# Optimization experiments

Hardware: AMD Instinct MI355X
Metric: run time of the kernel (lower is better)

The kernel has to match this reference:

```python
import jax, jax.numpy as jnp
import numpy as np
import math

HIDDEN = 256

def setup_inputs() -> dict:
    key = jax.random.key(0)
    ks = jax.random.split(key, 4)
    x = jax.random.normal(ks[0], (64, 1024, 32), dtype=jnp.float32)
    Wq = jax.random.normal(ks[1], (32, HIDDEN), dtype=jnp.float32) * (1.0 / math.sqrt(32))
    Wk = jax.random.normal(ks[2], (32, HIDDEN), dtype=jnp.float32) * (1.0 / math.sqrt(32))
    Wv = jax.random.normal(ks[3], (32, HIDDEN), dtype=jnp.float32) * (1.0 / math.sqrt(32))
    bq = jnp.zeros((HIDDEN,), jnp.float32)
    bk = jnp.zeros((HIDDEN,), jnp.float32)
    bv = jnp.zeros((HIDDEN,), jnp.float32)
    return {"x": x, "Wq": Wq, "bq": bq, "Wk": Wk, "bk": bk, "Wv": Wv, "bv": bv}

def reference(x, Wq, bq, Wk, bk, Wv, bv):
    # per-sample single-head attention; softmax FIRST, then divide by sqrt(hidden)
    Q = jnp.einsum('bsi,ih->bsh', x, Wq) + bq  # [B,S,H]
    K = jnp.einsum('bsi,ih->bsh', x, Wk) + bk
    V = jnp.einsum('bsi,ih->bsh', x, Wv) + bv
    scores = jnp.einsum('bqh,bkh->bqk', Q, K)  # [B,S,S]
    attn = jax.nn.softmax(scores, axis=-1) / jnp.sqrt(jnp.float32(Q.shape[-1]))
    Z = jnp.einsum('bqk,bkh->bqh', attn, V)
    return Z
```

## Files before the change

kernel.cpp:

```cpp
#include <hip/hip_runtime.h>
#include <math.h>

#define NB   64
#define SEQ  1024
#define DIN  32
#define HID  256
#define QT   128
#define KT   64
#define NKT  (SEQ/KT)
#define LOG2E 1.4426950408889634f

typedef float        f32x16 __attribute__((ext_vector_type(16)));
typedef short        s16x8  __attribute__((ext_vector_type(8)));
typedef _Float16     f16x8  __attribute__((ext_vector_type(8)));
typedef unsigned int u32x4v __attribute__((ext_vector_type(4)));
typedef unsigned int u32x2v __attribute__((ext_vector_type(2)));

#define MFMA32(A,B,C)  __builtin_amdgcn_mfma_f32_32x32x16_bf16(A,B,C,0,0,0)
#define MFMA32H(A,B,C) __builtin_amdgcn_mfma_f32_32x32x16_f16(A,B,C,0,0,0)

#define OFF_WVT  4224
#define OFF_A    24576
#define OFF_T    (OFF_A + 64*16*8192)
#define WS_NEED  ((size_t)OFF_T + 64*16*4096)

#define SETB(g,p) (((g)*2+(p))*12288)
#define ATS_OFF   49152
#define SMEM_SZ   (ATS_OFF + 4224)

__device__ __forceinline__ float ex2(float v) {
  return __builtin_amdgcn_exp2f(v);
}
__device__ __forceinline__ unsigned pk_bf16(float lo, float hi) {
  unsigned r;
  asm("v_cvt_pk_bf16_f32 %0, %1, %2" : "=v"(r) : "v"(lo), "v"(hi));
  return r;
}
__device__ __forceinline__ unsigned pkh(float a, float b) {
  return __builtin_bit_cast(unsigned, __builtin_amdgcn_cvt_pkrtz(a, b));
}
__device__ __forceinline__ void plswap(unsigned &vdst, unsigned &vsrc) {
  u32x2v r = __builtin_amdgcn_permlane32_swap(vdst, vsrc, false, false);
  vdst = r[0]; vsrc = r[1];
}
__device__ __forceinline__ float cross_max(float v) {
  u32x2v r = __builtin_amdgcn_permlane32_swap(__float_as_uint(v), __float_as_uint(v), false, false);
  return fmaxf(__uint_as_float(r[0]), __uint_as_float(r[1]));
}
__device__ __forceinline__ float cross_add(float v) {
  u32x2v r = __builtin_amdgcn_permlane32_swap(__float_as_uint(v), __float_as_uint(v), false, false);
  return __uint_as_float(r[0]) + __uint_as_float(r[1]);
}
__device__ __forceinline__ s16x8 frag4(unsigned a, unsigned b, unsigned c, unsigned d) {
  u32x4v t; t[0]=a; t[1]=b; t[2]=c; t[3]=d;
  return __builtin_bit_cast(s16x8, t);
}
__device__ __forceinline__ f16x8 frag4h(unsigned a, unsigned b, unsigned c, unsigned d) {
  u32x4v t; t[0]=a; t[1]=b; t[2]=c; t[3]=d;
  return __builtin_bit_cast(f16x8, t);
}
__device__ __forceinline__ f16x8 ldh(const void* p) {
  return __builtin_bit_cast(f16x8, *(const u32x4v*)p);
}
__device__ __forceinline__ unsigned bf16_hi_bits(float f) {
  unsigned ux = __float_as_uint(f);
  return (ux + 0x7fffu + ((ux >> 16) & 1u)) >> 16;
}
__device__ __forceinline__ unsigned pack_h2(float a, float b) {
  _Float16 ha = (_Float16)a, hb = (_Float16)b;
  return (unsigned)__builtin_bit_cast(unsigned short, ha) |
         ((unsigned)__builtin_bit_cast(unsigned short, hb) << 16);
}


__global__ __launch_bounds__(256) void pack2_kernel(
    const float* __restrict__ x,
    const float* __restrict__ Wq, const float* __restrict__ Wk,
    const float* __restrict__ bq, const float* __restrict__ Wv,
    char* __restrict__ ws) {
  __shared__ float xs[64 * 33];
  const int bid = blockIdx.x;
  const int t   = threadIdx.x;
  if (bid < 1024) {
    const int b = bid >> 4, kt = bid & 15;
    {
      const int r = t >> 2, c = (t & 3) * 8;
      const float* src = x + ((size_t)(b*SEQ + kt*KT + r))*DIN + c;
      float4 v0 = *(const float4*)src, v1 = *(const float4*)(src + 4);
      float* d = xs + r*33 + c;
      d[0]=v0.x; d[1]=v0.y; d[2]=v0.z; d[3]=v0.w;
      d[4]=v1.x; d[5]=v1.y; d[6]=v1.z; d[7]=v1.w;
    }
    __syncthreads();
    const int l = t & 63, f = t >> 6;
    const int w = l >> 5, lq = l & 31;
    {
      const int row = ((f&2)?32:0) + lq;
      const int d0  = ((f&1)?16:0) + 8*w;
      const float* vsrc = xs + row*33 + d0;
      unsigned hi[4], lo[4];
      #pragma unroll
      for (int j = 0; j < 4; ++j) {
        float a = vsrc[2*j], c2 = vsrc[2*j+1];
        _Float16 ha = (_Float16)a, hb = (_Float16)c2;
        hi[j] = (unsigned)__builtin_bit_cast(unsigned short, ha) |
                ((unsigned)__builtin_bit_cast(unsigned short, hb) << 16);
        lo[j] = pack_h2(a - (float)ha, c2 - (float)hb);
      }
      char* dst = ws + OFF_A + (size_t)bid*8192 + f*1024 + l*16;
      *(u32x4v*)dst          = (u32x4v){hi[0],hi[1],hi[2],hi[3]};
      *(u32x4v*)(dst + 4096) = (u32x4v){lo[0],lo[1],lo[2],lo[3]};
    }
    {
      const int k0 = 16*f + 8*w;
      unsigned hi[4];
      #pragma unroll
      for (int j = 0; j < 4; ++j)
        hi[j] = pack_h2(xs[(k0 + 2*j)*33 + lq], xs[(k0 + 2*j + 1)*33 + lq]);
      char* dst = ws + OFF_T + (size_t)bid*4096 + f*1024 + l*16;
      *(u32x4v*)dst = (u32x4v){hi[0],hi[1],hi[2],hi[3]};
    }
  } else {
    const int gid = (bid - 1024) * 256 + t;
    float* wsf = (float*)ws;
    if (gid < 1024) {
      int i = gid >> 5, j = gid & 31;
      const float* a  = Wq + j * HID;
      const float* b2 = Wk + i * HID;
      float a0=0.f,a1=0.f,a2=0.f,a3=0.f;
      for (int h = 0; h < HID; h += 8) {
        float4 x1 = *(const float4*)(a + h),  y1 = *(const float4*)(b2 + h);
        float4 x2 = *(const float4*)(a + h+4), y2 = *(const float4*)(b2 + h+4);
        a0 = fmaf(x1.x,y1.x,a0); a1 = fmaf(x1.y,y1.y,a1);
        a2 = fmaf(x1.z,y1.z,a2); a3 = fmaf(x1.w,y1.w,a3);
        a0 = fmaf(x2.x,y2.x,a0); a1 = fmaf(x2.y,y2.y,a1);
        a2 = fmaf(x2.z,y2.z,a2); a3 = fmaf(x2.w,y2.w,a3);
      }
      wsf[gid] = ((a0+a1)+(a2+a3)) * LOG2E;
    } else if (gid < 1056) {
      int i2 = gid - 1024;
      const float* b2 = Wk + i2 * HID;
      float acc = 0.f;
      for (int h = 0; h < HID; ++h) acc = fmaf(b2[h], bq[h], acc);
      wsf[1024 + i2] = acc * LOG2E;
    } else if (gid < 1056 + HID*16) {
      int e = gid - 1056;
      int h = e >> 4, d = e & 15;
      ((unsigned*)(ws + OFF_WVT))[e] = pkh(Wv[(2*d)*HID + h] * 0.0625f,
                                           Wv[(2*d+1)*HID + h] * 0.0625f);
    }
  }
}

__global__ __launch_bounds__(256, 4) void attn_fast(
    const float* __restrict__ x, const char* __restrict__ ws,
    const float* __restrict__ bv, float* __restrict__ out) {
  __shared__ __align__(16) char smem[18432];
  const int bid = blockIdx.x;
  const int vid = (bid & 7) * 256 + (bid >> 3);
  const int b   = vid >> 5;
  const int q0  = (vid & 31) * 32;
  const int t = threadIdx.x;
  const int wid = t>>6, lane = t&63, w = lane>>5, lq = lane&31;
  const int grp = wid;

  float* ATs = (float*)smem;
  float* Gs  = (float*)(smem + 4480);
  {
    const float* wsf = (const float*)ws;
    for (int e = t; e < 1024; e += 256) ATs[(e>>5)*33 + (e&31)] = wsf[e];
    if (t < 32) ATs[1056 + t] = wsf[1024 + t];
  }
  __syncthreads();
  {
    const int q = t >> 3, i0 = (t & 7) * 4;
    float xq[32];
    const float* xrow = x + (size_t)(b*SEQ + q0 + q) * DIN;
    #pragma unroll
    for (int c = 0; c < 8; ++c) {
      float4 v = *(const float4*)(xrow + c*4);
      xq[c*4+0]=v.x; xq[c*4+1]=v.y; xq[c*4+2]=v.z; xq[c*4+3]=v.w;
    }
    #pragma unroll
    for (int jo = 0; jo < 4; ++jo) {
      const int i = i0 + jo;
      const float* ar = ATs + i*33;
      float acc = ATs[1056 + i];
      #pragma unroll
      for (int j = 0; j < 32; ++j) acc = fmaf(xq[j], ar[j], acc);
      Gs[q*33 + i] = acc;
    }
  }
  __syncthreads();
  f16x8 G0h, G0l, G1h, G1l;
  {
    float g[16];
    #pragma unroll
    for (int ii = 0; ii < 16; ++ii) {
      const int i = 8*w + 16*(ii>>3) + (ii&7);
      g[ii] = Gs[lq*33 + i];
    }
    unsigned gh[8], gl[8];
    #pragma unroll
    for (int p = 0; p < 8; ++p) {
      float a = g[2*p], bb = g[2*p+1];
      _Float16 ha = (_Float16)a, hb = (_Float16)bb;
      gh[p] = (unsigned)__builtin_bit_cast(unsigned short, ha) |
              ((unsigned)__builtin_bit_cast(unsigned short, hb) << 16);
      gl[p] = pack_h2(a - (float)ha, bb - (float)hb);
    }
    G0h = frag4h(gh[0],gh[1],gh[2],gh[3]);
    G1h = frag4h(gh[4],gh[5],gh[6],gh[7]);
    G0l = frag4h(gl[0],gl[1],gl[2],gl[3]);
    G1l = frag4h(gl[4],gl[5],gl[6],gl[7]);
  }
  __syncthreads();

  f32x16 oacc;
  #pragma unroll
  for (int r = 0; r < 16; ++r) oacc[r] = 0.f;
  float m = -INFINITY, l = 0.f;

  const char* Ab = ws + OFF_A + (size_t)(b*16 + grp*4)*8192;
  const char* Tb = ws + OFF_T + (size_t)(b*16 + grp*4)*4096;
  const int lo16 = lane*16;

  #pragma unroll 2
  for (int j = 0; j < 4; ++j) {
    const char* A = Ab + j*8192;
    const char* T = Tb + j*4096;
    f16x8 ah0 = ldh(A + 0*1024 + lo16);
    f16x8 ah1 = ldh(A + 1*1024 + lo16);
    f16x8 ah2 = ldh(A + 2*1024 + lo16);
    f16x8 ah3 = ldh(A + 3*1024 + lo16);
    f16x8 al0 = ldh(A + 4096 + 0*1024 + lo16);
    f16x8 al1 = ldh(A + 4096 + 1*1024 + lo16);
    f16x8 al2 = ldh(A + 4096 + 2*1024 + lo16);
    f16x8 al3 = ldh(A + 4096 + 3*1024 + lo16);
    f16x8 at0 = ldh(T + 0*1024 + lo16);
    f16x8 at1 = ldh(T + 1*1024 + lo16);
    f16x8 at2 = ldh(T + 2*1024 + lo16);
    f16x8 at3 = ldh(T + 3*1024 + lo16);

    f32x16 sa0, sa1;
    #pragma unroll
    for (int r = 0; r < 16; ++r) { sa0[r] = 0.f; sa1[r] = 0.f; }
    sa0 = MFMA32H(ah0, G0h, sa0); sa0 = MFMA32H(ah0, G0l, sa0); sa0 = MFMA32H(al0, G0h, sa0);
    sa0 = MFMA32H(ah1, G1h, sa0); sa0 = MFMA32H(ah1, G1l, sa0); sa0 = MFMA32H(al1, G1h, sa0);
    sa1 = MFMA32H(ah2, G0h, sa1); sa1 = MFMA32H(ah2, G0l, sa1); sa1 = MFMA32H(al2, G0h, sa1);
    sa1 = MFMA32H(ah3, G1h, sa1); sa1 = MFMA32H(ah3, G1l, sa1); sa1 = MFMA32H(al3, G1h, sa1);

    float t0 = fmaxf(fmaxf(sa0[0], sa0[1]),  fmaxf(sa0[2],  sa0[3]));
    float t1 = fmaxf(fmaxf(sa0[4], sa0[5]),  fmaxf(sa0[6],  sa0[7]));
    float t2 = fmaxf(fmaxf(sa0[8], sa0[9]),  fmaxf(sa0[10], sa0[11]));
    float t3 = fmaxf(fmaxf(sa0[12],sa0[13]), fmaxf(sa0[14], sa0[15]));
    float t4 = fmaxf(fmaxf(sa1[0], sa1[1]),  fmaxf(sa1[2],  sa1[3]));
    float t5 = fmaxf(fmaxf(sa1[4], sa1[5]),  fmaxf(sa1[6],  sa1[7]));
    float t6 = fmaxf(fmaxf(sa1[8], sa1[9]),  fmaxf(sa1[10], sa1[11]));
    float t7 = fmaxf(fmaxf(sa1[12],sa1[13]), fmaxf(sa1[14], sa1[15]));
    float tm = fmaxf(fmaxf(fmaxf(t0,t1), fmaxf(t2,t3)),
                     fmaxf(fmaxf(t4,t5), fmaxf(t6,t7)));
    tm = cross_max(tm);
    if (!__all(tm - m <= 11.5415603f)) {
      float mn = fmaxf(m, tm);
      float alpha = ex2(m - mn);
      m = mn;
      l *= alpha;
      #pragma unroll
      for (int r = 0; r < 16; ++r) oacc[r] *= alpha;
    }
    #pragma unroll
    for (int r = 0; r < 16; ++r) { sa0[r] = ex2(sa0[r] - m); sa1[r] = ex2(sa1[r] - m); }
    float s0 = (sa0[0] + sa0[1])  + (sa0[2]  + sa0[3]);
    float s1 = (sa0[4] + sa0[5])  + (sa0[6]  + sa0[7]);
    float s2 = (sa0[8] + sa0[9])  + (sa0[10] + sa0[11]);
    float s3 = (sa0[12]+ sa0[13]) + (sa0[14] + sa0[15]);
    float s4 = (sa1[0] + sa1[1])  + (sa1[2]  + sa1[3]);
    float s5 = (sa1[4] + sa1[5])  + (sa1[6]  + sa1[7]);
    float s6 = (sa1[8] + sa1[9])  + (sa1[10] + sa1[11]);
    float s7 = (sa1[12]+ sa1[13]) + (sa1[14] + sa1[15]);
    float ps = ((s0+s1) + (s2+s3)) + ((s4+s5) + (s6+s7));
    ps = cross_add(ps);
    l += ps;

    {
      unsigned u0 = pkh(sa0[0], sa0[1]),  u1 = pkh(sa0[2], sa0[3]);
      unsigned v0 = pkh(sa0[4], sa0[5]),  v1 = pkh(sa0[6], sa0[7]);
      plswap(u0, v0); plswap(u1, v1);
      oacc = MFMA32H(at0, frag4h(u0, u1, v0, v1), oacc);

      unsigned u2 = pkh(sa0[8], sa0[9]),   u3 = pkh(sa0[10], sa0[11]);
      unsigned v2 = pkh(sa0[12], sa0[13]), v3 = pkh(sa0[14], sa0[15]);
      plswap(u2, v2); plswap(u3, v3);
      oacc = MFMA32H(at1, frag4h(u2, u3, v2, v3), oacc);

      unsigned u4 = pkh(sa1[0], sa1[1]),  u5 = pkh(sa1[2], sa1[3]);
      unsigned v4 = pkh(sa1[4], sa1[5]),  v5 = pkh(sa1[6], sa1[7]);
      plswap(u4, v4); plswap(u5, v5);
      oacc = MFMA32H(at2, frag4h(u4, u5, v4, v5), oacc);

      unsigned u6 = pkh(sa1[8], sa1[9]),   u7 = pkh(sa1[10], sa1[11]);
      unsigned v6 = pkh(sa1[12], sa1[13]), v7 = pkh(sa1[14], sa1[15]);
      plswap(u6, v6); plswap(u7, v7);
      oacc = MFMA32H(at3, frag4h(u6, u7, v6, v7), oacc);
    }
  }

  {
    float* base = (float*)smem;
    #pragma unroll
    for (int r = 0; r < 16; ++r) base[r*256 + t] = oacc[r];
    base[4096 + t] = m;
    base[4352 + t] = l;
    __syncthreads();
    #pragma unroll
    for (int og = 0; og < 4; ++og) {
      if (og == wid) continue;
      const int pt = (og<<6) | lane;
      float pm = base[4096 + pt], pl = base[4352 + pt];
      float mf = fmaxf(m, pm);
      float as = ex2(m - mf), ap = ex2(pm - mf);
      l = l * as + pl * ap;
      #pragma unroll
      for (int r = 0; r < 16; ++r)
        oacc[r] = oacc[r] * as + base[r*256 + pt] * ap;
      m = mf;
    }
    __syncthreads();
  }

  float inv = 1.0f / l;
  #pragma unroll
  for (int r = 0; r < 16; ++r) oacc[r] *= inv;
  f16x8 of0, of1;
  {
    unsigned u0 = pkh(oacc[0], oacc[1]),  u1 = pkh(oacc[2], oacc[3]);
    unsigned v0 = pkh(oacc[4], oacc[5]),  v1 = pkh(oacc[6], oacc[7]);
    plswap(u0, v0); plswap(u1, v1);
    of0 = frag4h(u0, u1, v0, v1);
    unsigned u2 = pkh(oacc[8], oacc[9]),   u3 = pkh(oacc[10], oacc[11]);
    unsigned v2 = pkh(oacc[12], oacc[13]), v3 = pkh(oacc[14], oacc[15]);
    plswap(u2, v2); plswap(u3, v3);
    of1 = frag4h(u2, u3, v2, v3);
  }
  const char* WvTb = ws + OFF_WVT;
  float* zb = (float*)(smem + wid * 4224);
  const size_t orow = ((size_t)b * SEQ + q0);
  #pragma unroll 1
  for (int mi = 0; mi < 2; ++mi) {
    const int mt = wid*2 + mi;
    const char* wp = WvTb + (mt*32 + lq)*64 + 16*w;
    f16x8 a0 = ldh(wp);
    f16x8 a1 = ldh(wp + 32);
    f32x16 z;
    #pragma unroll
    for (int r = 0; r < 16; ++r) z[r] = 0.f;
    z = MFMA32H(a0, of0, z);
    z = MFMA32H(a1, of1, z);
    #pragma unroll
    for (int r = 0; r < 16; ++r) {
      int hl = (r&3) + 8*(r>>2) + 4*w;
      zb[hl*33 + lq] = z[r];
    }
    asm volatile("s_waitcnt lgkmcnt(0)" ::: "memory");
    float bvv = bv[mt*32 + lq] * 0.0625f;
    #pragma unroll
    for (int jj = 0; jj < 16; ++jj) {
      int q = w*16 + jj;
      out[(orow + q)*HID + mt*32 + lq] = zb[lq*33 + q] + bvv;
    }
    asm volatile("s_waitcnt lgkmcnt(0)" ::: "memory");
  }
}


__global__ void precompute_kernel(const float* __restrict__ Wq, const float* __restrict__ Wk,
                                  const float* __restrict__ bq, const float* __restrict__ Wv,
                                  float* __restrict__ ws) {
  const int gid = blockIdx.x * 256 + threadIdx.x;
  if (gid < 1024) {
    int i = gid >> 5, j = gid & 31;
    const float* a  = Wq + j * HID;
    const float* b2 = Wk + i * HID;
    float a0=0.f,a1=0.f,a2=0.f,a3=0.f;
    for (int h = 0; h < HID; h += 8) {
      float4 x1 = *(const float4*)(a + h),  y1 = *(const float4*)(b2 + h);
      float4 x2 = *(const float4*)(a + h+4), y2 = *(const float4*)(b2 + h+4);
      a0 = fmaf(x1.x,y1.x,a0); a1 = fmaf(x1.y,y1.y,a1);
      a2 = fmaf(x1.z,y1.z,a2); a3 = fmaf(x1.w,y1.w,a3);
      a0 = fmaf(x2.x,y2.x,a0); a1 = fmaf(x2.y,y2.y,a1);
      a2 = fmaf(x2.z,y2.z,a2); a3 = fmaf(x2.w,y2.w,a3);
    }
    ws[gid] = (a0+a1)+(a2+a3);
  } else if (gid < 1056) {
    int i2 = gid - 1024;
    const float* b2 = Wk + i2 * HID;
    float acc = 0.f;
    for (int h = 0; h < HID; ++h) acc = fmaf(b2[h], bq[h], acc);
    ws[1024 + i2] = acc;
  } else if (gid < 1056 + HID*16) {
    int e = gid - 1056;
    int h = e >> 4, d = e & 15;
    ((unsigned*)((char*)ws + 4224))[e] = pk_bf16(Wv[(2*d)*HID + h], Wv[(2*d+1)*HID + h]);
  }
}

__global__ __launch_bounds__(512, 4) void attn_kernel(
    const float* __restrict__ x, const float* __restrict__ ws,
    const float* __restrict__ bv, float* __restrict__ out) {
  __shared__ __align__(16) char smem[SMEM_SZ];
  const int b    = blockIdx.y;
  const int q0   = blockIdx.x * QT;
  const int t    = threadIdx.x;
  const int grp  = t >> 8;
  const int ts   = t & 255;
  const int wid  = t >> 6;
  const int wq   = wid & 3;
  const int lane = t & 63;
  const int w    = lane >> 5;
  const int lq   = lane & 31;
  const float* xb = x + (size_t)b * SEQ * DIN;

  float* ATs = (float*)(smem + ATS_OFF);
  for (int e = t; e < 1056; e += 512) ATs[e] = ws[e];

  {
    const int sb = SETB(grp, 0);
    const int r = ts >> 2, s4 = ts & 3;
    const float* src = xb + (size_t)(grp * KT + r) * DIN + s4 * 8;
    float4 va = *(const float4*)src;
    float4 vb = *(const float4*)(src + 4);
    unsigned h0 = bf16_hi_bits(va.x) | (bf16_hi_bits(va.y) << 16);
    unsigned h1 = bf16_hi_bits(va.z) | (bf16_hi_bits(va.w) << 16);
    unsigned h2 = bf16_hi_bits(vb.x) | (bf16_hi_bits(vb.y) << 16);
    unsigned h3 = bf16_hi_bits(vb.z) | (bf16_hi_bits(vb.w) << 16);
    unsigned l0 = bf16_hi_bits(va.x - __uint_as_float(h0<<16)) | (bf16_hi_bits(va.y - __uint_as_float(h0 & 0xffff0000u)) << 16);
    unsigned l1 = bf16_hi_bits(va.z - __uint_as_float(h1<<16)) | (bf16_hi_bits(va.w - __uint_as_float(h1 & 0xffff0000u)) << 16);
    unsigned l2 = bf16_hi_bits(vb.x - __uint_as_float(h2<<16)) | (bf16_hi_bits(vb.y - __uint_as_float(h2 & 0xffff0000u)) << 16);
    unsigned l3 = bf16_hi_bits(vb.z - __uint_as_float(h3<<16)) | (bf16_hi_bits(vb.w - __uint_as_float(h3 & 0xffff0000u)) << 16);
    int off = r*64 + ((s4 ^ (r & 3)) << 4);
    *(u32x4v*)(smem + sb + off)        = (u32x4v){h0,h1,h2,h3};
    *(u32x4v*)(smem + sb + 4096 + off) = (u32x4v){l0,l1,l2,l3};
    const int ci = ts & 31, cr = (ts >> 5) * 8;
    const float* cs = xb + (size_t)(grp * KT + cr) * DIN + ci;
    float c0=cs[0], c1=cs[DIN], c2=cs[2*DIN], c3=cs[3*DIN];
    float c4=cs[4*DIN], c5=cs[5*DIN], c6=cs[6*DIN], c7=cs[7*DIN];
    unsigned t0 = pk_bf16(c0,c1), t1 = pk_bf16(c2,c3), t2 = pk_bf16(c4,c5), t3 = pk_bf16(c6,c7);
    int toff = sb + 8192 + ci*128 + (((ts>>5) ^ (ci & 7)) << 4);
    *(u32x4v*)(smem + toff) = (u32x4v){t0,t1,t2,t3};
  }
  __syncthreads();

  float g[16];
  {
    float xq[32];
    const float* xrow = xb + (size_t)(q0 + wq*32 + lq) * DIN;
    #pragma unroll
    for (int c = 0; c < 8; ++c) {
      float4 v = *(const float4*)(xrow + c*4);
      xq[c*4+0]=v.x; xq[c*4+1]=v.y; xq[c*4+2]=v.z; xq[c*4+3]=v.w;
    }
    #pragma unroll
    for (int ii = 0; ii < 16; ++ii) {
      const int i = 8*w + 16*(ii>>3) + (ii&7);
      const float* ar = ATs + i*32;
      float acc = ATs[1024 + i];
      #pragma unroll
      for (int j = 0; j < 8; ++j) {
        float4 av = *(const float4*)(ar + j*4);
        acc = fmaf(xq[j*4+0], av.x, acc);
        acc = fmaf(xq[j*4+1], av.y, acc);
        acc = fmaf(xq[j*4+2], av.z, acc);
        acc = fmaf(xq[j*4+3], av.w, acc);
      }
      g[ii] = acc;
    }
  }
  s16x8 G0h, G0l, G1h, G1l;
  {
    unsigned gh[2][4], gl[2][4];
    #pragma unroll
    for (int Ks = 0; Ks < 2; ++Ks)
      #pragma unroll
      for (int d = 0; d < 4; ++d) {
        float ga = g[Ks*8 + 2*d], gb = g[Ks*8 + 2*d + 1];
        unsigned hp = bf16_hi_bits(ga) | (bf16_hi_bits(gb) << 16);
        unsigned lp = bf16_hi_bits(ga - __uint_as_float(hp<<16)) |
                      (bf16_hi_bits(gb - __uint_as_float(hp & 0xffff0000u)) << 16);
        gh[Ks][d] = hp; gl[Ks][d] = lp;
      }
    G0h = frag4(gh[0][0],gh[0][1],gh[0][2],gh[0][3]);
    G0l = frag4(gl[0][0],gl[0][1],gl[0][2],gl[0][3]);
    G1h = frag4(gh[1][0],gh[1][1],gh[1][2],gh[1][3]);
    G1l = frag4(gl[1][0],gl[1][1],gl[1][2],gl[1][3]);
  }

  f32x16 oacc;
  #pragma unroll
  for (int r = 0; r < 16; ++r) oacc[r] = 0.f;
  float m = -INFINITY, l = 0.f;

  for (int j = 0; j < NKT/2; ++j) {
    const bool hn = (j + 1 < NKT/2);
    float4 va, vb;
    float c0=0,c1=0,c2=0,c3=0,c4=0,c5=0,c6=0,c7=0;
    if (hn) {
      const int ktn = 2*(j+1) + grp;
      const int r = ts >> 2, s4 = ts & 3;
      const float* src = xb + (size_t)(ktn*KT + r) * DIN + s4*8;
      va = *(const float4*)src;
      vb = *(const float4*)(src + 4);
      const int ci = ts & 31, cr = (ts >> 5) * 8;
      const float* cs = xb + (size_t)(ktn*KT + cr) * DIN + ci;
      c0=cs[0]; c1=cs[DIN]; c2=cs[2*DIN]; c3=cs[3*DIN];
      c4=cs[4*DIN]; c5=cs[5*DIN]; c6=cs[6*DIN]; c7=cs[7*DIN];
    }

    const int sb = SETB(grp, j & 1);
    const char* bh = smem + sb;
    const char* bl = smem + sb + 4096;
    const int co0 = ((w    ) ^ (lq & 3)) << 4;
    const int co1 = ((w + 2) ^ (lq & 3)) << 4;
    s16x8 ah00 = *(const s16x8*)(bh + lq*64 + co0);
    s16x8 ah01 = *(const s16x8*)(bh + lq*64 + co1);
    s16x8 al00 = *(const s16x8*)(bl + lq*64 + co0);
    s16x8 al01 = *(const s16x8*)(bl + lq*64 + co1);
    s16x8 ah10 = *(const s16x8*)(bh + (32+lq)*64 + co0);
    s16x8 ah11 = *(const s16x8*)(bh + (32+lq)*64 + co1);
    s16x8 al10 = *(const s16x8*)(bl + (32+lq)*64 + co0);
    s16x8 al11 = *(const s16x8*)(bl + (32+lq)*64 + co1);
    f32x16 sa0, sa1;
    #pragma unroll
    for (int r = 0; r < 16; ++r) { sa0[r] = 0.f; sa1[r] = 0.f; }
    sa0 = MFMA32(ah00, G0h, sa0); sa0 = MFMA32(ah00, G0l, sa0); sa0 = MFMA32(al00, G0h, sa0);
    sa0 = MFMA32(ah01, G1h, sa0); sa0 = MFMA32(ah01, G1l, sa0); sa0 = MFMA32(al01, G1h, sa0);
    sa1 = MFMA32(ah10, G0h, sa1); sa1 = MFMA32(ah10, G0l, sa1); sa1 = MFMA32(al10, G0h, sa1);
    sa1 = MFMA32(ah11, G1h, sa1); sa1 = MFMA32(ah11, G1l, sa1); sa1 = MFMA32(al11, G1h, sa1);

    float tm = sa0[0];
    #pragma unroll
    for (int r = 1; r < 16; ++r) tm = fmaxf(tm, sa0[r]);
    #pragma unroll
    for (int r = 0; r < 16; ++r) tm = fmaxf(tm, sa1[r]);
    tm = cross_max(tm);
    float mn = fmaxf(m, tm);
    float alpha = __expf(m - mn);
    m = mn;
    float ps = 0.f;
    #pragma unroll
    for (int r = 0; r < 16; ++r) { float p = __expf(sa0[r] - mn); sa0[r] = p; ps += p; }
    #pragma unroll
    for (int r = 0; r < 16; ++r) { float p = __expf(sa1[r] - mn); sa1[r] = p; ps += p; }
    ps = cross_add(ps);
    l = l * alpha + ps;
    #pragma unroll
    for (int r = 0; r < 16; ++r) oacc[r] *= alpha;

    const char* bt = smem + sb + 8192;
    {
      unsigned u0 = pk_bf16(sa0[0], sa0[1]),  u1 = pk_bf16(sa0[2], sa0[3]);
      unsigned v0 = pk_bf16(sa0[4], sa0[5]),  v1 = pk_bf16(sa0[6], sa0[7]);
      plswap(u0, v0); plswap(u1, v1);
      s16x8 at0 = *(const s16x8*)(bt + lq*128 + (((0 + w) ^ (lq & 7)) << 4));
      oacc = MFMA32(at0, frag4(u0, u1, v0, v1), oacc);

      unsigned u2 = pk_bf16(sa0[8], sa0[9]),   u3 = pk_bf16(sa0[10], sa0[11]);
      unsigned v2 = pk_bf16(sa0[12], sa0[13]), v3 = pk_bf16(sa0[14], sa0[15]);
      plswap(u2, v2); plswap(u3, v3);
      s16x8 at1 = *(const s16x8*)(bt + lq*128 + (((2 + w) ^ (lq & 7)) << 4));
      oacc = MFMA32(at1, frag4(u2, u3, v2, v3), oacc);

      unsigned u4 = pk_bf16(sa1[0], sa1[1]),  u5 = pk_bf16(sa1[2], sa1[3]);
      unsigned v4 = pk_bf16(sa1[4], sa1[5]),  v5 = pk_bf16(sa1[6], sa1[7]);
      plswap(u4, v4); plswap(u5, v5);
      s16x8 at2 = *(const s16x8*)(bt + lq*128 + (((4 + w) ^ (lq & 7)) << 4));
      oacc = MFMA32(at2, frag4(u4, u5, v4, v5), oacc);

      unsigned u6 = pk_bf16(sa1[8], sa1[9]),   u7 = pk_bf16(sa1[10], sa1[11]);
      unsigned v6 = pk_bf16(sa1[12], sa1[13]), v7 = pk_bf16(sa1[14], sa1[15]);
      plswap(u6, v6); plswap(u7, v7);
      s16x8 at3 = *(const s16x8*)(bt + lq*128 + (((6 + w) ^ (lq & 7)) << 4));
      oacc = MFMA32(at3, frag4(u6, u7, v6, v7), oacc);
    }

    if (hn) {
      const int nsb = SETB(grp, (j+1) & 1);
      const int r = ts >> 2, s4 = ts & 3;
      unsigned h0 = bf16_hi_bits(va.x) | (bf16_hi_bits(va.y) << 16);
      unsigned h1 = bf16_hi_bits(va.z) | (bf16_hi_bits(va.w) << 16);
      unsigned h2 = bf16_hi_bits(vb.x) | (bf16_hi_bits(vb.y) << 16);
      unsigned h3 = bf16_hi_bits(vb.z) | (bf16_hi_bits(vb.w) << 16);
      unsigned l0 = bf16_hi_bits(va.x - __uint_as_float(h0<<16)) | (bf16_hi_bits(va.y - __uint_as_float(h0 & 0xffff0000u)) << 16);
      unsigned l1 = bf16_hi_bits(va.z - __uint_as_float(h1<<16)) | (bf16_hi_bits(va.w - __uint_as_float(h1 & 0xffff0000u)) << 16);
      unsigned l2 = bf16_hi_bits(vb.x - __uint_as_float(h2<<16)) | (bf16_hi_bits(vb.y - __uint_as_float(h2 & 0xffff0000u)) << 16);
      unsigned l3 = bf16_hi_bits(vb.z - __uint_as_float(h3<<16)) | (bf16_hi_bits(vb.w - __uint_as_float(h3 & 0xffff0000u)) << 16);
      int off = r*64 + ((s4 ^ (r & 3)) << 4);
      *(u32x4v*)(smem + nsb + off)        = (u32x4v){h0,h1,h2,h3};
      *(u32x4v*)(smem + nsb + 4096 + off) = (u32x4v){l0,l1,l2,l3};
      const int ci = ts & 31;
      unsigned t0 = pk_bf16(c0,c1), t1 = pk_bf16(c2,c3), t2 = pk_bf16(c4,c5), t3 = pk_bf16(c6,c7);
      int toff = nsb + 8192 + ci*128 + (((ts>>5) ^ (ci & 7)) << 4);
      *(u32x4v*)(smem + toff) = (u32x4v){t0,t1,t2,t3};
    }
    __syncthreads();
  }

  {
    float* ms = (float*)(smem + grp*20480 + (((wq<<6) | lane) * 80));
    *(float4*)(ms + 0)  = (float4){oacc[0],  oacc[1],  oacc[2],  oacc[3]};
    *(float4*)(ms + 4)  = (float4){oacc[4],  oacc[5],  oacc[6],  oacc[7]};
    *(float4*)(ms + 8)  = (float4){oacc[8],  oacc[9],  oacc[10], oacc[11]};
    *(float4*)(ms + 12) = (float4){oacc[12], oacc[13], oacc[14], oacc[15]};
    ms[16] = m; ms[17] = l;
    __syncthreads();
    const float* pp = (const float*)(smem + (1-grp)*20480 + (((wq<<6) | lane) * 80));
    float4 p0 = *(const float4*)(pp + 0);
    float4 p1 = *(const float4*)(pp + 4);
    float4 p2 = *(const float4*)(pp + 8);
    float4 p3 = *(const float4*)(pp + 12);
    float pm = pp[16], pl = pp[17];
    float mf = fmaxf(m, pm);
    float as = __expf(m - mf), ap = __expf(pm - mf);
    l = l * as + pl * ap;
    float po[16] = {p0.x,p0.y,p0.z,p0.w, p1.x,p1.y,p1.z,p1.w,
                    p2.x,p2.y,p2.z,p2.w, p3.x,p3.y,p3.z,p3.w};
    #pragma unroll
    for (int r = 0; r < 16; ++r) oacc[r] = oacc[r] * as + po[r] * ap;
    __syncthreads();
  }

  float inv = 1.0f / (16.0f * l);
  #pragma unroll
  for (int r = 0; r < 16; ++r) oacc[r] *= inv;
  s16x8 of0, of1;
  {
    unsigned u0 = pk_bf16(oacc[0], oacc[1]),  u1 = pk_bf16(oacc[2], oacc[3]);
    unsigned v0 = pk_bf16(oacc[4], oacc[5]),  v1 = pk_bf16(oacc[6], oacc[7]);
    plswap(u0, v0); plswap(u1, v1);
    of0 = frag4(u0, u1, v0, v1);
    unsigned u2 = pk_bf16(oacc[8], oacc[9]),   u3 = pk_bf16(oacc[10], oacc[11]);
    unsigned v2 = pk_bf16(oacc[12], oacc[13]), v3 = pk_bf16(oacc[14], oacc[15]);
    plswap(u2, v2); plswap(u3, v3);
    of1 = frag4(u2, u3, v2, v3);
  }
  const char* WvTb = (const char*)ws + 4224;
  float* zb = (float*)(smem + wid * 4224);
  const size_t orow = ((size_t)b * SEQ + q0 + wq*32);
  #pragma unroll 1
  for (int mi = 0; mi < 4; ++mi) {
    const int mt = grp*4 + mi;
    const char* wp = WvTb + (mt*32 + lq)*64 + 16*w;
    s16x8 a0 = *(const s16x8*)wp;
    s16x8 a1 = *(const s16x8*)(wp + 32);
    f32x16 z;
    #pragma unroll
    for (int r = 0; r < 16; ++r) z[r] = 0.f;
    z = MFMA32(a0, of0, z);
    z = MFMA32(a1, of1, z);
    #pragma unroll
    for (int r = 0; r < 16; ++r) {
      int hl = (r&3) + 8*(r>>2) + 4*w;
      zb[hl*33 + lq] = z[r];
    }
    asm volatile("s_waitcnt lgkmcnt(0)" ::: "memory");
    float bvv = bv[mt*32 + lq] * 0.0625f;
    #pragma unroll
    for (int jj = 0; jj < 16; ++jj) {
      int q = w*16 + jj;
      out[(orow + q)*HID + mt*32 + lq] = zb[lq*33 + q] + bvv;
    }
    asm volatile("s_waitcnt lgkmcnt(0)" ::: "memory");
  }
}

extern "C" void kernel_launch(void* const* d_in, const int* in_sizes, int n_in,
                              void* d_out, int out_size, void* d_ws, size_t ws_size,
                              hipStream_t stream) {
  (void)in_sizes; (void)n_in; (void)out_size;
  const float* x  = (const float*)d_in[0];
  const float* Wq = (const float*)d_in[1];
  const float* bq = (const float*)d_in[2];
  const float* Wk = (const float*)d_in[3];
  const float* Wv = (const float*)d_in[5];
  const float* bv = (const float*)d_in[6];
  float* out = (float*)d_out;
  float* ws  = (float*)d_ws;

  if (ws_size >= WS_NEED) {
    pack2_kernel<<<1048, 256, 0, stream>>>(x, Wq, Wk, bq, Wv, (char*)ws);
    attn_fast<<<2048, 256, 0, stream>>>(x, (const char*)ws, bv, out);
  } else {
    precompute_kernel<<<24, 256, 0, stream>>>(Wq, Wk, bq, Wv, ws);
    attn_kernel<<<dim3(SEQ/QT, NB), 512, 0, stream>>>(x, ws, bv, out);
  }
}
```

Measured before the change: 58.08 us.

## Process two 32-query sub-tiles per block to reuse loaded K/V fragments

Each block now handles 64 queries as two 32-row sub-tiles with separate online-softmax state, so every A/T fragment loaded from global memory feeds two sets of score and PV MFMAs. The grid is halved, shared memory doubles for the cross-wave merge, and launch bounds drop to 3 blocks per CU to allow the extra register pressure. The aim is to halve global K/V traffic per query, at the cost of fewer resident waves and more registers.

```diff
diff --git a/kernel.cpp b/kernel.cpp
--- a/kernel.cpp
+++ b/kernel.cpp
@@ -152,14 +152,66 @@
   }
 }
 
-__global__ __launch_bounds__(256, 4) void attn_fast(
+#define SM_PV(sa0, sa1, mvar, lvar, oaccvar)                                     \
+  {                                                                              \
+    float t0 = fmaxf(fmaxf(sa0[0], sa0[1]),  fmaxf(sa0[2],  sa0[3]));            \
+    float t1 = fmaxf(fmaxf(sa0[4], sa0[5]),  fmaxf(sa0[6],  sa0[7]));            \
+    float t2 = fmaxf(fmaxf(sa0[8], sa0[9]),  fmaxf(sa0[10], sa0[11]));           \
+    float t3 = fmaxf(fmaxf(sa0[12],sa0[13]), fmaxf(sa0[14], sa0[15]));           \
+    float t4 = fmaxf(fmaxf(sa1[0], sa1[1]),  fmaxf(sa1[2],  sa1[3]));            \
+    float t5 = fmaxf(fmaxf(sa1[4], sa1[5]),  fmaxf(sa1[6],  sa1[7]));            \
+    float t6 = fmaxf(fmaxf(sa1[8], sa1[9]),  fmaxf(sa1[10], sa1[11]));           \
+    float t7 = fmaxf(fmaxf(sa1[12],sa1[13]), fmaxf(sa1[14], sa1[15]));           \
+    float tm = fmaxf(fmaxf(fmaxf(t0,t1), fmaxf(t2,t3)),                          \
+                     fmaxf(fmaxf(t4,t5), fmaxf(t6,t7)));                         \
+    tm = cross_max(tm);                                                          \
+    if (!__all(tm - mvar <= 11.5415603f)) {                                      \
+      float mn = fmaxf(mvar, tm);                                                \
+      float alpha = ex2(mvar - mn);                                              \
+      mvar = mn;                                                                 \
+      lvar *= alpha;                                                             \
+      _Pragma("unroll")                                                          \
+      for (int r = 0; r < 16; ++r) oaccvar[r] *= alpha;                          \
+    }                                                                            \
+    _Pragma("unroll")                                                            \
+    for (int r = 0; r < 16; ++r) { sa0[r] = ex2(sa0[r] - mvar); sa1[r] = ex2(sa1[r] - mvar); } \
+    float s0 = (sa0[0] + sa0[1])  + (sa0[2]  + sa0[3]);                          \
+    float s1 = (sa0[4] + sa0[5])  + (sa0[6]  + sa0[7]);                          \
+    float s2 = (sa0[8] + sa0[9])  + (sa0[10] + sa0[11]);                         \
+    float s3 = (sa0[12]+ sa0[13]) + (sa0[14] + sa0[15]);                         \
+    float s4 = (sa1[0] + sa1[1])  + (sa1[2]  + sa1[3]);                          \
+    float s5 = (sa1[4] + sa1[5])  + (sa1[6]  + sa1[7]);                          \
+    float s6 = (sa1[8] + sa1[9])  + (sa1[10] + sa1[11]);                         \
+    float s7 = (sa1[12]+ sa1[13]) + (sa1[14] + sa1[15]);                         \
+    float ps = ((s0+s1) + (s2+s3)) + ((s4+s5) + (s6+s7));                        \
+    ps = cross_add(ps);                                                          \
+    lvar += ps;                                                                  \
+    unsigned u0 = pkh(sa0[0], sa0[1]),  u1 = pkh(sa0[2], sa0[3]);                \
+    unsigned v0 = pkh(sa0[4], sa0[5]),  v1 = pkh(sa0[6], sa0[7]);                \
+    plswap(u0, v0); plswap(u1, v1);                                              \
+    unsigned u2 = pkh(sa0[8], sa0[9]),   u3 = pkh(sa0[10], sa0[11]);             \
+    unsigned v2 = pkh(sa0[12], sa0[13]), v3 = pkh(sa0[14], sa0[15]);             \
+    plswap(u2, v2); plswap(u3, v3);                                              \
+    unsigned u4 = pkh(sa1[0], sa1[1]),  u5 = pkh(sa1[2], sa1[3]);                \
+    unsigned v4 = pkh(sa1[4], sa1[5]),  v5 = pkh(sa1[6], sa1[7]);                \
+    plswap(u4, v4); plswap(u5, v5);                                              \
+    unsigned u6 = pkh(sa1[8], sa1[9]),   u7 = pkh(sa1[10], sa1[11]);             \
+    unsigned v6 = pkh(sa1[12], sa1[13]), v7 = pkh(sa1[14], sa1[15]);             \
+    plswap(u6, v6); plswap(u7, v7);                                              \
+    oaccvar = MFMA32H(at0, frag4h(u0, u1, v0, v1), oaccvar);                     \
+    oaccvar = MFMA32H(at1, frag4h(u2, u3, v2, v3), oaccvar);                     \
+    oaccvar = MFMA32H(at2, frag4h(u4, u5, v4, v5), oaccvar);                     \
+    oaccvar = MFMA32H(at3, frag4h(u6, u7, v6, v7), oaccvar);                     \
+  }
+
+__global__ __launch_bounds__(256, 3) void attn_fast(
     const float* __restrict__ x, const char* __restrict__ ws,
     const float* __restrict__ bv, float* __restrict__ out) {
-  __shared__ __align__(16) char smem[18432];
+  __shared__ __align__(16) char smem[36864];
   const int bid = blockIdx.x;
-  const int vid = (bid & 7) * 256 + (bid >> 3);
-  const int b   = vid >> 5;
-  const int q0  = (vid & 31) * 32;
+  const int vid = (bid & 7) * 128 + (bid >> 3);
+  const int b   = vid >> 4;
+  const int q0  = (vid & 15) * 64;
   const int t = threadIdx.x;
   const int wid = t>>6, lane = t&63, w = lane>>5, lq = lane&31;
   const int grp = wid;
@@ -173,7 +225,7 @@
   }
   __syncthreads();
   {
-    const int q = t >> 3, i0 = (t & 7) * 4;
+    const int q = t >> 2, i0 = (t & 3) * 8;
     float xq[32];
     const float* xrow = x + (size_t)(b*SEQ + q0 + q) * DIN;
     #pragma unroll
@@ -182,7 +234,7 @@
       xq[c*4+0]=v.x; xq[c*4+1]=v.y; xq[c*4+2]=v.z; xq[c*4+3]=v.w;
     }
     #pragma unroll
-    for (int jo = 0; jo < 4; ++jo) {
+    for (int jo = 0; jo < 8; ++jo) {
       const int i = i0 + jo;
       const float* ar = ATs + i*33;
       float acc = ATs[1056 + i];
@@ -192,15 +244,15 @@
     }
   }
   __syncthreads();
-  f16x8 G0h, G0l, G1h, G1l;
+  f16x8 G0h_a, G0l_a, G1h_a, G1l_a, G0h_b, G0l_b, G1h_b, G1l_b;
   {
     float g[16];
+    unsigned gh[8], gl[8];
     #pragma unroll
     for (int ii = 0; ii < 16; ++ii) {
       const int i = 8*w + 16*(ii>>3) + (ii&7);
       g[ii] = Gs[lq*33 + i];
     }
-    unsigned gh[8], gl[8];
     #pragma unroll
     for (int p = 0; p < 8; ++p) {
       float a = g[2*p], bb = g[2*p+1];
@@ -209,17 +261,34 @@
               ((unsigned)__builtin_bit_cast(unsigned short, hb) << 16);
       gl[p] = pack_h2(a - (float)ha, bb - (float)hb);
     }
-    G0h = frag4h(gh[0],gh[1],gh[2],gh[3]);
-    G1h = frag4h(gh[4],gh[5],gh[6],gh[7]);
-    G0l = frag4h(gl[0],gl[1],gl[2],gl[3]);
-    G1l = frag4h(gl[4],gl[5],gl[6],gl[7]);
+    G0h_a = frag4h(gh[0],gh[1],gh[2],gh[3]);
+    G1h_a = frag4h(gh[4],gh[5],gh[6],gh[7]);
+    G0l_a = frag4h(gl[0],gl[1],gl[2],gl[3]);
+    G1l_a = frag4h(gl[4],gl[5],gl[6],gl[7]);
+    #pragma unroll
+    for (int ii = 0; ii < 16; ++ii) {
+      const int i = 8*w + 16*(ii>>3) + (ii&7);
+      g[ii] = Gs[(32+lq)*33 + i];
+    }
+    #pragma unroll
+    for (int p = 0; p < 8; ++p) {
+      float a = g[2*p], bb = g[2*p+1];
+      _Float16 ha = (_Float16)a, hb = (_Float16)bb;
+      gh[p] = (unsigned)__builtin_bit_cast(unsigned short, ha) |
+              ((unsigned)__builtin_bit_cast(unsigned short, hb) << 16);
+      gl[p] = pack_h2(a - (float)ha, bb - (float)hb);
+    }
+    G0h_b = frag4h(gh[0],gh[1],gh[2],gh[3]);
+    G1h_b = frag4h(gh[4],gh[5],gh[6],gh[7]);
+    G0l_b = frag4h(gl[0],gl[1],gl[2],gl[3]);
+    G1l_b = frag4h(gl[4],gl[5],gl[6],gl[7]);
   }
   __syncthreads();
 
-  f32x16 oacc;
+  f32x16 oaccA, oaccB;
   #pragma unroll
-  for (int r = 0; r < 16; ++r) oacc[r] = 0.f;
-  float m = -INFINITY, l = 0.f;
+  for (int r = 0; r < 16; ++r) { oaccA[r] = 0.f; oaccB[r] = 0.f; }
+  float mA = -INFINITY, lA = 0.f, mB = -INFINITY, lB = 0.f;
 
   const char* Ab = ws + OFF_A + (size_t)(b*16 + grp*4)*8192;
   const char* Tb = ws + OFF_T + (size_t)(b*16 + grp*4)*4096;
@@ -242,134 +311,115 @@
     f16x8 at2 = ldh(T + 2*1024 + lo16);
     f16x8 at3 = ldh(T + 3*1024 + lo16);
 
-    f32x16 sa0, sa1;
-    #pragma unroll
-    for (int r = 0; r < 16; ++r) { sa0[r] = 0.f; sa1[r] = 0.f; }
-    sa0 = MFMA32H(ah0, G0h, sa0); sa0 = MFMA32H(ah0, G0l, sa0); sa0 = MFMA32H(al0, G0h, sa0);
-    sa0 = MFMA32H(ah1, G1h, sa0); sa0 = MFMA32H(ah1, G1l, sa0); sa0 = MFMA32H(al1, G1h, sa0);
-    sa1 = MFMA32H(ah2, G0h, sa1); sa1 = MFMA32H(ah2, G0l, sa1); sa1 = MFMA32H(al2, G0h, sa1);
-    sa1 = MFMA32H(ah3, G1h, sa1); sa1 = MFMA32H(ah3, G1l, sa1); sa1 = MFMA32H(al3, G1h, sa1);
-
-    float t0 = fmaxf(fmaxf(sa0[0], sa0[1]),  fmaxf(sa0[2],  sa0[3]));
-    float t1 = fmaxf(fmaxf(sa0[4], sa0[5]),  fmaxf(sa0[6],  sa0[7]));
-    float t2 = fmaxf(fmaxf(sa0[8], sa0[9]),  fmaxf(sa0[10], sa0[11]));
-    float t3 = fmaxf(fmaxf(sa0[12],sa0[13]), fmaxf(sa0[14], sa0[15]));
-    float t4 = fmaxf(fmaxf(sa1[0], sa1[1]),  fmaxf(sa1[2],  sa1[3]));
-    float t5 = fmaxf(fmaxf(sa1[4], sa1[5]),  fmaxf(sa1[6],  sa1[7]));
-    float t6 = fmaxf(fmaxf(sa1[8], sa1[9]),  fmaxf(sa1[10], sa1[11]));
-    float t7 = fmaxf(fmaxf(sa1[12],sa1[13]), fmaxf(sa1[14], sa1[15]));
-    float tm = fmaxf(fmaxf(fmaxf(t0,t1), fmaxf(t2,t3)),
-                     fmaxf(fmaxf(t4,t5), fmaxf(t6,t7)));
-    tm = cross_max(tm);
-    if (!__all(tm - m <= 11.5415603f)) {
-      float mn = fmaxf(m, tm);
-      float alpha = ex2(m - mn);
-      m = mn;
-      l *= alpha;
-      #pragma unroll
-      for (int r = 0; r < 16; ++r) oacc[r] *= alpha;
-    }
-    #pragma unroll
-    for (int r = 0; r < 16; ++r) { sa0[r] = ex2(sa0[r] - m); sa1[r] = ex2(sa1[r] - m); }
-    float s0 = (sa0[0] + sa0[1])  + (sa0[2]  + sa0[3]);
-    float s1 = (sa0[4] + sa0[5])  + (sa0[6]  + sa0[7]);
-    float s2 = (sa0[8] + sa0[9])  + (sa0[10] + sa0[11]);
-    float s3 = (sa0[12]+ sa0[13]) + (sa0[14] + sa0[15]);
-    float s4 = (sa1[0] + sa1[1])  + (sa1[2]  + sa1[3]);
-    float s5 = (sa1[4] + sa1[5])  + (sa1[6]  + sa1[7]);
-    float s6 = (sa1[8] + sa1[9])  + (sa1[10] + sa1[11]);
-    float s7 = (sa1[12]+ sa1[13]) + (sa1[14] + sa1[15]);
-    float ps = ((s0+s1) + (s2+s3)) + ((s4+s5) + (s6+s7));
-    ps = cross_add(ps);
-    l += ps;
-
     {
-      unsigned u0 = pkh(sa0[0], sa0[1]),  u1 = pkh(sa0[2], sa0[3]);
-      unsigned v0 = pkh(sa0[4], sa0[5]),  v1 = pkh(sa0[6], sa0[7]);
-      plswap(u0, v0); plswap(u1, v1);
-      oacc = MFMA32H(at0, frag4h(u0, u1, v0, v1), oacc);
-
-      unsigned u2 = pkh(sa0[8], sa0[9]),   u3 = pkh(sa0[10], sa0[11]);
-      unsigned v2 = pkh(sa0[12], sa0[13]), v3 = pkh(sa0[14], sa0[15]);
-      plswap(u2, v2); plswap(u3, v3);
-      oacc = MFMA32H(at1, frag4h(u2, u3, v2, v3), oacc);
-
-      unsigned u4 = pkh(sa1[0], sa1[1]),  u5 = pkh(sa1[2], sa1[3]);
-      unsigned v4 = pkh(sa1[4], sa1[5]),  v5 = pkh(sa1[6], sa1[7]);
-      plswap(u4, v4); plswap(u5, v5);
-      oacc = MFMA32H(at2, frag4h(u4, u5, v4, v5), oacc);
-
-      unsigned u6 = pkh(sa1[8], sa1[9]),   u7 = pkh(sa1[10], sa1[11]);
-      unsigned v6 = pkh(sa1[12], sa1[13]), v7 = pkh(sa1[14], sa1[15]);
-      plswap(u6, v6); plswap(u7, v7);
-      oacc = MFMA32H(at3, frag4h(u6, u7, v6, v7), oacc);
+      f32x16 sa0, sa1;
+      #pragma unroll
+      for (int r = 0; r < 16; ++r) { sa0[r] = 0.f; sa1[r] = 0.f; }
+      sa0 = MFMA32H(ah0, G0h_a, sa0); sa0 = MFMA32H(ah0, G0l_a, sa0); sa0 = MFMA32H(al0, G0h_a, sa0);
+      sa0 = MFMA32H(ah1, G1h_a, sa0); sa0 = MFMA32H(ah1, G1l_a, sa0); sa0 = MFMA32H(al1, G1h_a, sa0);
+      sa1 = MFMA32H(ah2, G0h_a, sa1); sa1 = MFMA32H(ah2, G0l_a, sa1); sa1 = MFMA32H(al2, G0h_a, sa1);
+      sa1 = MFMA32H(ah3, G1h_a, sa1); sa1 = MFMA32H(ah3, G1l_a, sa1); sa1 = MFMA32H(al3, G1h_a, sa1);
+      SM_PV(sa0, sa1, mA, lA, oaccA)
+    }
+    {
+      f32x16 sa0, sa1;
+      #pragma unroll
+      for (int r = 0; r < 16; ++r) { sa0[r] = 0.f; sa1[r] = 0.f; }
+      sa0 = MFMA32H(ah0, G0h_b, sa0); sa0 = MFMA32H(ah0, G0l_b, sa0); sa0 = MFMA32H(al0, G0h_b, sa0);
+      sa0 = MFMA32H(ah1, G1h_b, sa0); sa0 = MFMA32H(ah1, G1l_b, sa0); sa0 = MFMA32H(al1, G1h_b, sa0);
+      sa1 = MFMA32H(ah2, G0h_b, sa1); sa1 = MFMA32H(ah2, G0l_b, sa1); sa1 = MFMA32H(al2, G0h_b, sa1);
+      sa1 = MFMA32H(ah3, G1h_b, sa1); sa1 = MFMA32H(ah3, G1l_b, sa1); sa1 = MFMA32H(al3, G1h_b, sa1);
+      SM_PV(sa0, sa1, mB, lB, oaccB)
     }
   }
 
   {
     float* base = (float*)smem;
     #pragma unroll
-    for (int r = 0; r < 16; ++r) base[r*256 + t] = oacc[r];
-    base[4096 + t] = m;
-    base[4352 + t] = l;
+    for (int r = 0; r < 16; ++r) base[r*256 + t] = oaccA[r];
+    #pragma unroll
+    for (int r = 0; r < 16; ++r) base[(16+r)*256 + t] = oaccB[r];
+    base[8192 + t]  = mA;
+    base[8448 + t]  = lA;
+    base[8704 + t]  = mB;
+    base[8960 + t]  = lB;
     __syncthreads();
     #pragma unroll
     for (int og = 0; og < 4; ++og) {
       if (og == wid) continue;
       const int pt = (og<<6) | lane;
-      float pm = base[4096 + pt], pl = base[4352 + pt];
-      float mf = fmaxf(m, pm);
-      float as = ex2(m - mf), ap = ex2(pm - mf);
-      l = l * as + pl * ap;
-      #pragma unroll
-      for (int r = 0; r < 16; ++r)
-        oacc[r] = oacc[r] * as + base[r*256 + pt] * ap;
-      m = mf;
+      {
+        float pm = base[8192 + pt], pl = base[8448 + pt];
+        float mf = fmaxf(mA, pm);
+        float as = ex2(mA - mf), ap = ex2(pm - mf);
+        lA = lA * as + pl * ap;
+        #pragma unroll
+        for (int r = 0; r < 16; ++r)
+          oaccA[r] = oaccA[r] * as + base[r*256 + pt] * ap;
+        mA = mf;
+      }
+      {
+        float pm = base[8704 + pt], pl = base[8960 + pt];
+        float mf = fmaxf(mB, pm);
+        float as = ex2(mB - mf), ap = ex2(pm - mf);
+        lB = lB * as + pl * ap;
+        #pragma unroll
+        for (int r = 0; r < 16; ++r)
+          oaccB[r] = oaccB[r] * as + base[(16+r)*256 + pt] * ap;
+        mB = mf;
+      }
     }
     __syncthreads();
   }
 
-  float inv = 1.0f / l;
-  #pragma unroll
-  for (int r = 0; r < 16; ++r) oacc[r] *= inv;
-  f16x8 of0, of1;
-  {
-    unsigned u0 = pkh(oacc[0], oacc[1]),  u1 = pkh(oacc[2], oacc[3]);
-    unsigned v0 = pkh(oacc[4], oacc[5]),  v1 = pkh(oacc[6], oacc[7]);
-    plswap(u0, v0); plswap(u1, v1);
-    of0 = frag4h(u0, u1, v0, v1);
-    unsigned u2 = pkh(oacc[8], oacc[9]),   u3 = pkh(oacc[10], oacc[11]);
-    unsigned v2 = pkh(oacc[12], oacc[13]), v3 = pkh(oacc[14], oacc[15]);
-    plswap(u2, v2); plswap(u3, v3);
-    of1 = frag4h(u2, u3, v2, v3);
-  }
   const char* WvTb = ws + OFF_WVT;
   float* zb = (float*)(smem + wid * 4224);
-  const size_t orow = ((size_t)b * SEQ + q0);
   #pragma unroll 1
-  for (int mi = 0; mi < 2; ++mi) {
-    const int mt = wid*2 + mi;
-    const char* wp = WvTb + (mt*32 + lq)*64 + 16*w;
-    f16x8 a0 = ldh(wp);
-    f16x8 a1 = ldh(wp + 32);
-    f32x16 z;
-    #pragma unroll
-    for (int r = 0; r < 16; ++r) z[r] = 0.f;
-    z = MFMA32H(a0, of0, z);
-    z = MFMA32H(a1, of1, z);
-    #pragma unroll
-    for (int r = 0; r < 16; ++r) {
-      int hl = (r&3) + 8*(r>>2) + 4*w;
-      zb[hl*33 + lq] = z[r];
-    }
-    asm volatile("s_waitcnt lgkmcnt(0)" ::: "memory");
-    float bvv = bv[mt*32 + lq] * 0.0625f;
-    #pragma unroll
-    for (int jj = 0; jj < 16; ++jj) {
-      int q = w*16 + jj;
-      out[(orow + q)*HID + mt*32 + lq] = zb[lq*33 + q] + bvv;
-    }
-    asm volatile("s_waitcnt lgkmcnt(0)" ::: "memory");
+  for (int sub = 0; sub < 2; ++sub) {
+    f32x16 oac;
+    float lv;
+    if (sub == 0) { oac = oaccA; lv = lA; }
+    else          { oac = oaccB; lv = lB; }
+    float inv = 1.0f / lv;
+    #pragma unroll
+    for (int r = 0; r < 16; ++r) oac[r] *= inv;
+    f16x8 of0, of1;
+    {
+      unsigned u0 = pkh(oac[0], oac[1]),  u1 = pkh(oac[2], oac[3]);
+      unsigned v0 = pkh(oac[4], oac[5]),  v1 = pkh(oac[6], oac[7]);
+      plswap(u0, v0); plswap(u1, v1);
+      of0 = frag4h(u0, u1, v0, v1);
+      unsigned u2 = pkh(oac[8], oac[9]),   u3 = pkh(oac[10], oac[11]);
+      unsigned v2 = pkh(oac[12], oac[13]), v3 = pkh(oac[14], oac[15]);
+      plswap(u2, v2); plswap(u3, v3);
+      of1 = frag4h(u2, u3, v2, v3);
+    }
+    const size_t orow = ((size_t)b * SEQ + q0 + sub*32);
+    #pragma unroll 1
+    for (int mi = 0; mi < 2; ++mi) {
+      const int mt = wid*2 + mi;
+      const char* wp = WvTb + (mt*32 + lq)*64 + 16*w;
+      f16x8 a0 = ldh(wp);
+      f16x8 a1 = ldh(wp + 32);
+      f32x16 z;
+      #pragma unroll
+      for (int r = 0; r < 16; ++r) z[r] = 0.f;
+      z = MFMA32H(a0, of0, z);
+      z = MFMA32H(a1, of1, z);
+      #pragma unroll
+      for (int r = 0; r < 16; ++r) {
+        int hl = (r&3) + 8*(r>>2) + 4*w;
+        zb[hl*33 + lq] = z[r];
+      }
+      asm volatile("s_waitcnt lgkmcnt(0)" ::: "memory");
+      float bvv = bv[mt*32 + lq] * 0.0625f;
+      #pragma unroll
+      for (int jj = 0; jj < 16; ++jj) {
+        int q = w*16 + jj;
+        out[(orow + q)*HID + mt*32 + lq] = zb[lq*33 + q] + bvv;
+      }
+      asm volatile("s_waitcnt lgkmcnt(0)" ::: "memory");
+    }
   }
 }
 
@@ -688,7 +738,7 @@
 
   if (ws_size >= WS_NEED) {
     pack2_kernel<<<1048, 256, 0, stream>>>(x, Wq, Wk, bq, Wv, (char*)ws);
-    attn_fast<<<2048, 256, 0, stream>>>(x, (const char*)ws, bv, out);
+    attn_fast<<<1024, 256, 0, stream>>>(x, (const char*)ws, bv, out);
   } else {
     precompute_kernel<<<24, 256, 0, stream>>>(Wq, Wk, bq, Wv, ws);
     attn_kernel<<<dim3(SEQ/QT, NB), 512, 0, stream>>>(x, ws, bv, out);
```

Measured after the change: 60.93 us. 1.05x slower.
